# Performance work log

Hardware: AMD Instinct MI355X
Metric: run time of the kernel (lower is better)

## Reference

```python
import jax, jax.numpy as jnp
import numpy as np

B, C, H, W = 8, 64, 256, 256
K = 3  # num_experts in CondConv2D


def setup_inputs() -> dict:
    key = jax.random.key(0)
    ks = jax.random.split(key, 10)
    s = 0.05
    return {
        "x":    jax.random.normal(ks[0], (B, C, H, W), jnp.float32),
        # CondConv2D #1: depthwise 5x5, pad 2, dil 1
        "w0":   jax.random.normal(ks[1], (K, C, 1, 5, 5), jnp.float32) * s,
        "b0":   jax.random.normal(ks[2], (C,), jnp.float32) * s,
        "r0_w": jax.random.normal(ks[3], (K, C), jnp.float32) * s,
        "r0_b": jnp.zeros((K,), jnp.float32),
        # CondConv2D #2: depthwise 7x7, pad 9, dil 3
        "w1":   jax.random.normal(ks[4], (K, C, 1, 7, 7), jnp.float32) * s,
        "b1":   jax.random.normal(ks[5], (C,), jnp.float32) * s,
        "r1_w": jax.random.normal(ks[6], (K, C), jnp.float32) * s,
        "r1_b": jnp.zeros((K,), jnp.float32),
        # conv1: 1x1 pointwise
        "wp":   jax.random.normal(ks[7], (C, C), jnp.float32) * s,
        "bp":   jnp.zeros((C,), jnp.float32),
    }


def cond_dwconv(x, weight, bias, rw, rb, pad, dil):
    """Per-sample expert-mixed depthwise conv (CondConv with groups=C).
    x: [B,C,H,W]; weight: [K,C,1,ks,ks]; rw: [K,C], rb: [K]."""
    b, c, h, w = x.shape
    pooled = x.mean(axis=(2, 3))                      # [B,C] adaptive avg pool to 1x1
    r = jax.nn.sigmoid(pooled @ rw.T + rb)            # [B,K] routing weights
    wk = jnp.einsum('bk,kcihw->bcihw', r, weight)     # [B,C,1,ks,ks] mixed kernels
    ksz = weight.shape[-1]
    # batch-folded grouped conv: fold B into channel/group dim
    out = jax.lax.conv_general_dilated(
        x.reshape(1, b * c, h, w),
        wk.reshape(b * c, 1, ksz, ksz),
        window_strides=(1, 1),
        padding=[(pad, pad), (pad, pad)],
        rhs_dilation=(dil, dil),
        feature_group_count=b * c,
        dimension_numbers=('NCHW', 'OIHW', 'NCHW'))
    return out.reshape(b, c, h, w) + bias[None, :, None, None]


def reference(x, w0, b0, r0_w, r0_b, w1, b1, r1_w, r1_b, wp, bp):
    attn = jax.nn.gelu(cond_dwconv(x, w0, b0, r0_w, r0_b, pad=2, dil=1), approximate=False)
    attn = jax.nn.gelu(cond_dwconv(attn, w1, b1, r1_w, r1_b, pad=9, dil=3), approximate=False)
    attn = jnp.einsum('bchw,oc->bohw', attn, wp) + bp[None, :, None, None]  # 1x1 conv
    return x * attn
```

## Files before the change

### kernel.cpp

```cpp
#include <hip/hip_runtime.h>
#include <hip/hip_fp16.h>

#define HW 65536
#define PW 256
#define C7SD 85

__device__ __forceinline__ float gelu_f(float v) {
    float ax = fabsf(v) * 0.7071067811865476f;
    float t  = 1.0f / (1.0f + 0.3275911f * ax);
    float p  = t * (0.254829592f + t * (-0.284496736f + t * (1.421413741f
             + t * (-1.453152027f + t * 1.061405429f))));
    float e  = 1.0f - p * __expf(-ax * ax);
    e = copysignf(e, v);
    return 0.5f * v * (1.0f + e);
}

__device__ __forceinline__ unsigned pack2h(float a, float b) {
    __half2 h = __floats2half2_rn(a, b);
    return *reinterpret_cast<unsigned*>(&h);
}

__device__ __forceinline__ float sgpr_f(float v) {
    union { float f; int i; } u;
    u.f = v;
    u.i = __builtin_amdgcn_readfirstlane(u.i);
    return u.f;
}

__device__ __forceinline__ void fma_mix_h(float& acc, float w, unsigned h2, int sel) {
    if (sel == 0)
        asm("v_fma_mix_f32 %0, %1, %2, %0 op_sel:[0,0,0] op_sel_hi:[0,1,0]"
            : "+v"(acc) : "v"(w), "v"(h2));
    else
        asm("v_fma_mix_f32 %0, %1, %2, %0 op_sel:[0,1,0] op_sel_hi:[0,1,0]"
            : "+v"(acc) : "v"(w), "v"(h2));
}

__device__ __forceinline__ void dot2_h(float& acc, unsigned wpk, unsigned pr) {
    asm("v_dot2_f32_f16 %0, %1, %2, %0" : "+v"(acc) : "s"(wpk), "v"(pr));
}
__device__ __forceinline__ void dot2_hv(float& acc, unsigned wpk, unsigned pr) {
    asm("v_dot2_f32_f16 %0, %1, %2, %0" : "+v"(acc) : "v"(wpk), "v"(pr));
}

__global__ __launch_bounds__(256) void k_pool_x(const float* __restrict__ x,
                                                float* __restrict__ partial) {
    __shared__ float red[256];
    const int t = threadIdx.x;
    const int blk = blockIdx.x;
    const float* p = x + (size_t)blk * 16384;
    float s = 0.f;
    #pragma unroll
    for (int i = 0; i < 16; ++i) {
        float4 v = *reinterpret_cast<const float4*>(p + (i * 256 + t) * 4);
        s += v.x + v.y + v.z + v.w;
    }
    red[t] = s;
    __syncthreads();
    for (int off = 128; off > 0; off >>= 1) {
        if (t < off) red[t] += red[t + off];
        __syncthreads();
    }
    if (t == 0) partial[blk] = red[0];
}

__device__ __forceinline__ void route_block(const float* __restrict__ partial,
                                            const float* __restrict__ rw,
                                            const float* __restrict__ rb,
                                            const float* __restrict__ wexp,
                                            int b, int c, int taps, int t,
                                            float* pool_s, float* r_s, float* w_s) {
    if (t < 64) {
        float s = 0.f;
        #pragma unroll
        for (int q = 0; q < 4; ++q) s += partial[(b * 64 + t) * 4 + q];
        pool_s[t] = s * (1.0f / 65536.0f);
    }
    __syncthreads();
    if (t < 3) {
        float z = rb[t];
        #pragma unroll
        for (int i = 0; i < 64; ++i) z += pool_s[i] * rw[t * 64 + i];
        r_s[t] = 1.0f / (1.0f + expf(-z));
    }
    __syncthreads();
    if (t < taps) {
        w_s[t] = r_s[0] * wexp[(0 * 64 + c) * taps + t] +
                 r_s[1] * wexp[(1 * 64 + c) * taps + t] +
                 r_s[2] * wexp[(2 * 64 + c) * taps + t];
    }
    __syncthreads();
}

__global__ __launch_bounds__(256) void k_conv5(const float* __restrict__ x,
                                               const float* __restrict__ partial,
                                               const float* __restrict__ rw,
                                               const float* __restrict__ rb,
                                               const float* __restrict__ wexp,
                                               const float* __restrict__ bias,
                                               __half* __restrict__ attn0,
                                               float* __restrict__ tilesum) {
    __shared__ float red[256];
    __shared__ float pool_s[64];
    __shared__ float r_s[3];
    __shared__ float w_s[25];
    const int blk = blockIdx.x;
    const int plane = blk >> 2;
    const int tile = blk & 3;
    const int b = plane >> 6;
    const int c = plane & 63;
    const int oy0 = (tile >> 1) << 7;
    const int ox0 = (tile & 1) << 7;
    const int t = threadIdx.x;
    const int ox = ox0 + ((t & 15) << 3);
    const int oy = oy0 + ((t >> 4) << 3);
    const float* xp = x + (size_t)plane * HW;

    route_block(partial, rw, rb, wexp, b, c, 25, t, pool_s, r_s, w_s);
    float w[25];
    #pragma unroll
    for (int i = 0; i < 25; ++i) w[i] = sgpr_f(w_s[i]);

    float acc[8][8];
    #pragma unroll
    for (int i = 0; i < 8; ++i)
        #pragma unroll
        for (int j = 0; j < 8; ++j) acc[i][j] = 0.f;

    #pragma unroll
    for (int r = 0; r < 12; ++r) {
        const int gy = oy - 2 + r;
        if (gy >= 0 && gy < 256) {
            const float* rp = xp + gy * PW + ox;
            float buf[16];
            float4 v;
            if (ox > 0) v = *reinterpret_cast<const float4*>(rp - 4);
            else        v = make_float4(0.f, 0.f, 0.f, 0.f);
            buf[0] = v.x; buf[1] = v.y; buf[2] = v.z; buf[3] = v.w;
            v = *reinterpret_cast<const float4*>(rp);
            buf[4] = v.x; buf[5] = v.y; buf[6] = v.z; buf[7] = v.w;
            v = *reinterpret_cast<const float4*>(rp + 4);
            buf[8] = v.x; buf[9] = v.y; buf[10] = v.z; buf[11] = v.w;
            if (ox < 248) v = *reinterpret_cast<const float4*>(rp + 8);
            else          v = make_float4(0.f, 0.f, 0.f, 0.f);
            buf[12] = v.x; buf[13] = v.y; buf[14] = v.z; buf[15] = v.w;
            #pragma unroll
            for (int i = 0; i < 8; ++i) {
                const int d = r - i;
                if (d >= 0 && d <= 4) {
                    #pragma unroll
                    for (int dx = 0; dx < 5; ++dx) {
                        const float wv = w[d * 5 + dx];
                        #pragma unroll
                        for (int j = 0; j < 8; ++j)
                            acc[i][j] += wv * buf[j + dx + 2];
                    }
                }
            }
        }
    }
    const float bs = bias[c];
    float lsum = 0.f;
    __half* op = attn0 + (size_t)plane * HW;
    #pragma unroll
    for (int i = 0; i < 8; ++i) {
        float g[8];
        #pragma unroll
        for (int j = 0; j < 8; ++j) {
            g[j] = gelu_f(acc[i][j] + bs);
            lsum += g[j];
        }
        uint4 st;
        st.x = pack2h(g[0], g[1]); st.y = pack2h(g[2], g[3]);
        st.z = pack2h(g[4], g[5]); st.w = pack2h(g[6], g[7]);
        *reinterpret_cast<uint4*>(op + (oy + i) * PW + ox) = st;
    }
    red[t] = lsum;
    __syncthreads();
    for (int off = 128; off > 0; off >>= 1) {
        if (t < off) red[t] += red[t + off];
        __syncthreads();
    }
    if (t == 0) tilesum[blk] = red[0];
}

__global__ __launch_bounds__(256, 3) void k_conv7(const __half* __restrict__ a0,
                                                  const float* __restrict__ tilesum,
                                                  const float* __restrict__ rw,
                                                  const float* __restrict__ rb,
                                                  const float* __restrict__ wexp,
                                                  const float* __restrict__ bias,
                                                  __half* __restrict__ attn1) {
    __shared__ unsigned lds[82 * C7SD];
    __shared__ float pool_s[64];
    __shared__ float r_s[3];
    __shared__ float w_s[49];
    const int blk = blockIdx.x;
    const int plane = blk >> 3;
    const int tile = blk & 7;
    const int b = plane >> 6;
    const int c = plane & 63;
    const int oy0 = (tile >> 1) << 6;
    const int ox0 = (tile & 1) << 7;
    const int t = threadIdx.x;
    const __half* ap = a0 + (size_t)plane * HW;

    const uint4 z4 = make_uint4(0u, 0u, 0u, 0u);
    #pragma unroll
    for (int it = 0; it < 7; ++it) {
        const int idx = it * 256 + t;
        if (idx < 1722) {
            const int lr = idx / 21;
            const int c8 = idx - lr * 21;
            const int gy = oy0 - 9 + lr;
            const int gx = ox0 - 16 + (c8 << 3);
            uint4 v = z4;
            if ((unsigned)gy < 256u && (unsigned)gx < 256u)
                v = *reinterpret_cast<const uint4*>(ap + gy * PW + gx);
            unsigned* wp = &lds[lr * C7SD + (c8 << 2)];
            wp[0] = v.x; wp[1] = v.y; wp[2] = v.z; wp[3] = v.w;
        }
    }

    route_block(tilesum, rw, rb, wexp, b, c, 49, t, pool_s, r_s, w_s);
    unsigned wpk[21];
    #pragma unroll
    for (int p = 0; p < 3; ++p)
        #pragma unroll
        for (int dxi = 0; dxi < 7; ++dxi)
            wpk[p * 7 + dxi] = (unsigned)__builtin_amdgcn_readfirstlane(
                (int)pack2h(w_s[(2 * p) * 7 + dxi], w_s[(2 * p + 1) * 7 + dxi]));
    float wt[7];
    #pragma unroll
    for (int i = 0; i < 7; ++i) wt[i] = sgpr_f(w_s[42 + i]);
    __syncthreads();

    const int tx = t & 3, ty = t >> 2;
    const int ox = tx << 5;
    float acc[32];
    #pragma unroll
    for (int j = 0; j < 32; ++j) acc[j] = 0.f;

    #pragma unroll
    for (int p = 0; p < 3; ++p) {
        const int rA = ty + 6 * p;
        const unsigned* lA = &lds[rA * C7SD + (tx << 4)];
        const unsigned* lB = &lds[(rA + 3) * C7SD + (tx << 4)];
        unsigned hA[32], hB[32];
        #pragma unroll
        for (int i = 0; i < 32; ++i) hA[i] = lA[i];
        #pragma unroll
        for (int i = 0; i < 32; ++i) hB[i] = lB[i];
        unsigned pr[50];
        #pragma unroll
        for (int i = 0; i < 50; ++i) {
            const int s = i + 7, k = s >> 1;
            pr[i] = __builtin_amdgcn_perm(hB[k], hA[k],
                                          (s & 1) ? 0x07060302u : 0x05040100u);
        }
        #pragma unroll
        for (int dxi = 0; dxi < 7; ++dxi) {
            const unsigned wp = wpk[p * 7 + dxi];
            #pragma unroll
            for (int j = 0; j < 32; ++j)
                dot2_h(acc[j], wp, pr[3 * dxi + j]);
        }
    }
    {
        const unsigned* lp = &lds[(ty + 18) * C7SD + (tx << 4)];
        unsigned hbuf[32];
        #pragma unroll
        for (int i = 0; i < 32; ++i) hbuf[i] = lp[i];
        #pragma unroll
        for (int dxi = 0; dxi < 7; ++dxi) {
            const float wv = wt[dxi];
            const int o = 7 + 3 * dxi;
            #pragma unroll
            for (int j = 0; j < 32; ++j) {
                const int h = o + j;
                fma_mix_h(acc[j], wv, hbuf[h >> 1], h & 1);
            }
        }
    }

    const float bs = bias[c];
    __half* op = attn1 + (size_t)plane * HW + (size_t)(oy0 + ty) * PW + ox0 + ox;
    #pragma unroll
    for (int q = 0; q < 4; ++q) {
        float g[8];
        #pragma unroll
        for (int j = 0; j < 8; ++j) g[j] = gelu_f(acc[q * 8 + j] + bs);
        uint4 st;
        st.x = pack2h(g[0], g[1]); st.y = pack2h(g[2], g[3]);
        st.z = pack2h(g[4], g[5]); st.w = pack2h(g[6], g[7]);
        *reinterpret_cast<uint4*>(op + (q << 3)) = st;
    }
}

__global__ __launch_bounds__(256) void k_mix(const __half* __restrict__ attn1,
                                             const float* __restrict__ wpm,
                                             const float* __restrict__ bp,
                                             const float* __restrict__ x,
                                             float* __restrict__ out) {
    __shared__ __half A_s[64][128];
    __shared__ unsigned w2_s[32][64];
    const int t = threadIdx.x;
    const int blk = blockIdx.x;
    const int b = blk >> 9;
    const int p0g = (blk & 511) << 7;
    #pragma unroll
    for (int it = 0; it < 4; ++it) {
        const int idx = it * 256 + t;
        const int row = idx >> 4;
        const int off = (idx & 15) << 3;
        uint4 u = *reinterpret_cast<const uint4*>(attn1 + (size_t)(b * 64 + row) * HW + p0g + off);
        *reinterpret_cast<uint4*>(&A_s[row][off]) = u;
    }
    #pragma unroll
    for (int j = 0; j < 8; ++j) {
        const int idx = j * 256 + t;
        const int oo = idx >> 5;
        const int cc2 = idx & 31;
        w2_s[cc2][oo] = pack2h(wpm[oo * 64 + 2 * cc2], wpm[oo * 64 + 2 * cc2 + 1]);
    }
    __syncthreads();
    const int o0 = (t >> 4) << 2;
    const int p0 = (t & 15) << 3;
    float acc[4][8];
    #pragma unroll
    for (int i = 0; i < 4; ++i)
        #pragma unroll
        for (int j = 0; j < 8; ++j) acc[i][j] = 0.f;
    #pragma unroll 4
    for (int cc2 = 0; cc2 < 32; ++cc2) {
        uint4 a0 = *reinterpret_cast<const uint4*>(&A_s[2 * cc2][p0]);
        uint4 a1 = *reinterpret_cast<const uint4*>(&A_s[2 * cc2 + 1][p0]);
        const unsigned a0w[4] = {a0.x, a0.y, a0.z, a0.w};
        const unsigned a1w[4] = {a1.x, a1.y, a1.z, a1.w};
        unsigned pr[8];
        #pragma unroll
        for (int j = 0; j < 8; ++j)
            pr[j] = __builtin_amdgcn_perm(a1w[j >> 1], a0w[j >> 1],
                                          (j & 1) ? 0x07060302u : 0x05040100u);
        uint4 wv0 = *reinterpret_cast<const uint4*>(&w2_s[cc2][o0]);
        const unsigned wv[4] = {wv0.x, wv0.y, wv0.z, wv0.w};
        #pragma unroll
        for (int oo = 0; oo < 4; ++oo) {
            const unsigned wvv = wv[oo];
            #pragma unroll
            for (int pp = 0; pp < 8; ++pp)
                dot2_hv(acc[oo][pp], wvv, pr[pp]);
        }
    }
    #pragma unroll
    for (int oo = 0; oo < 4; ++oo) {
        const int o = o0 + oo;
        const float bb = bp[o];
        const size_t base = (size_t)(b * 64 + o) * HW + p0g + p0;
        float4 x0 = *reinterpret_cast<const float4*>(x + base);
        float4 x1 = *reinterpret_cast<const float4*>(x + base + 4);
        float4 r0, r1;
        r0.x = x0.x * (acc[oo][0] + bb); r0.y = x0.y * (acc[oo][1] + bb);
        r0.z = x0.z * (acc[oo][2] + bb); r0.w = x0.w * (acc[oo][3] + bb);
        r1.x = x1.x * (acc[oo][4] + bb); r1.y = x1.y * (acc[oo][5] + bb);
        r1.z = x1.z * (acc[oo][6] + bb); r1.w = x1.w * (acc[oo][7] + bb);
        *reinterpret_cast<float4*>(out + base) = r0;
        *reinterpret_cast<float4*>(out + base + 4) = r1;
    }
}

extern "C" void kernel_launch(void* const* d_in, const int* in_sizes, int n_in,
                              void* d_out, int out_size, void* d_ws, size_t ws_size,
                              hipStream_t stream) {
    const float* x   = (const float*)d_in[0];
    const float* w0  = (const float*)d_in[1];
    const float* b0  = (const float*)d_in[2];
    const float* r0w = (const float*)d_in[3];
    const float* r0b = (const float*)d_in[4];
    const float* w1  = (const float*)d_in[5];
    const float* b1  = (const float*)d_in[6];
    const float* r1w = (const float*)d_in[7];
    const float* r1b = (const float*)d_in[8];
    const float* wpm = (const float*)d_in[9];
    const float* bp  = (const float*)d_in[10];
    float* out = (float*)d_out;

    char* ws = (char*)d_ws;
    __half* attn0   = (__half*)(ws);
    __half* attn1   = (__half*)(ws + 67108864);
    float* partial0 = (float*)(ws + 134217728);
    float* tilesum1 = (float*)(ws + 134217728 + 8192);

    k_pool_x<<<2048, 256, 0, stream>>>(x, partial0);
    k_conv5<<<2048, 256, 0, stream>>>(x, partial0, r0w, r0b, w0, b0, attn0, tilesum1);
    k_conv7<<<4096, 256, 0, stream>>>(attn0, tilesum1, r1w, r1b, w1, b1, attn1);
    k_mix<<<4096, 256, 0, stream>>>(attn1, wpm, bp, x, out);
}
```

Before: 227.7 us.

## Rewrite 5x5 conv to stage fp16 tiles in LDS and use packed dot2

```diff
diff --git a/kernel.cpp b/kernel.cpp
--- a/kernel.cpp
+++ b/kernel.cpp
@@ -4,6 +4,7 @@
 #define HW 65536
 #define PW 256
 #define C7SD 85
+#define C5SD 73
 
 __device__ __forceinline__ float gelu_f(float v) {
     float ax = fabsf(v) * 0.7071067811865476f;
@@ -68,12 +69,11 @@
                                             const float* __restrict__ rw,
                                             const float* __restrict__ rb,
                                             const float* __restrict__ wexp,
-                                            int b, int c, int taps, int t,
+                                            int b, int c, int taps, int parts, int t,
                                             float* pool_s, float* r_s, float* w_s) {
     if (t < 64) {
         float s = 0.f;
-        #pragma unroll
-        for (int q = 0; q < 4; ++q) s += partial[(b * 64 + t) * 4 + q];
+        for (int q = 0; q < parts; ++q) s += partial[(b * 64 + t) * parts + q];
         pool_s[t] = s * (1.0f / 65536.0f);
     }
     __syncthreads();
@@ -92,88 +92,126 @@
     __syncthreads();
 }
 
-__global__ __launch_bounds__(256) void k_conv5(const float* __restrict__ x,
-                                               const float* __restrict__ partial,
-                                               const float* __restrict__ rw,
-                                               const float* __restrict__ rb,
-                                               const float* __restrict__ wexp,
-                                               const float* __restrict__ bias,
-                                               __half* __restrict__ attn0,
-                                               float* __restrict__ tilesum) {
+__global__ __launch_bounds__(256, 3) void k_conv5(const float* __restrict__ x,
+                                                  const float* __restrict__ partial,
+                                                  const float* __restrict__ rw,
+                                                  const float* __restrict__ rb,
+                                                  const float* __restrict__ wexp,
+                                                  const float* __restrict__ bias,
+                                                  __half* __restrict__ attn0,
+                                                  float* __restrict__ tilesum) {
+    __shared__ unsigned lds[68 * C5SD];
     __shared__ float red[256];
     __shared__ float pool_s[64];
     __shared__ float r_s[3];
     __shared__ float w_s[25];
     const int blk = blockIdx.x;
-    const int plane = blk >> 2;
-    const int tile = blk & 3;
+    const int plane = blk >> 3;
+    const int tile = blk & 7;
     const int b = plane >> 6;
     const int c = plane & 63;
-    const int oy0 = (tile >> 1) << 7;
+    const int oy0 = (tile >> 1) << 6;
     const int ox0 = (tile & 1) << 7;
     const int t = threadIdx.x;
-    const int ox = ox0 + ((t & 15) << 3);
-    const int oy = oy0 + ((t >> 4) << 3);
     const float* xp = x + (size_t)plane * HW;
 
-    route_block(partial, rw, rb, wexp, b, c, 25, t, pool_s, r_s, w_s);
-    float w[25];
-    #pragma unroll
-    for (int i = 0; i < 25; ++i) w[i] = sgpr_f(w_s[i]);
-
-    float acc[8][8];
-    #pragma unroll
-    for (int i = 0; i < 8; ++i)
-        #pragma unroll
-        for (int j = 0; j < 8; ++j) acc[i][j] = 0.f;
-
-    #pragma unroll
-    for (int r = 0; r < 12; ++r) {
-        const int gy = oy - 2 + r;
-        if (gy >= 0 && gy < 256) {
-            const float* rp = xp + gy * PW + ox;
-            float buf[16];
-            float4 v;
-            if (ox > 0) v = *reinterpret_cast<const float4*>(rp - 4);
-            else        v = make_float4(0.f, 0.f, 0.f, 0.f);
-            buf[0] = v.x; buf[1] = v.y; buf[2] = v.z; buf[3] = v.w;
-            v = *reinterpret_cast<const float4*>(rp);
-            buf[4] = v.x; buf[5] = v.y; buf[6] = v.z; buf[7] = v.w;
-            v = *reinterpret_cast<const float4*>(rp + 4);
-            buf[8] = v.x; buf[9] = v.y; buf[10] = v.z; buf[11] = v.w;
-            if (ox < 248) v = *reinterpret_cast<const float4*>(rp + 8);
-            else          v = make_float4(0.f, 0.f, 0.f, 0.f);
-            buf[12] = v.x; buf[13] = v.y; buf[14] = v.z; buf[15] = v.w;
-            #pragma unroll
-            for (int i = 0; i < 8; ++i) {
-                const int d = r - i;
-                if (d >= 0 && d <= 4) {
-                    #pragma unroll
-                    for (int dx = 0; dx < 5; ++dx) {
-                        const float wv = w[d * 5 + dx];
-                        #pragma unroll
-                        for (int j = 0; j < 8; ++j)
-                            acc[i][j] += wv * buf[j + dx + 2];
-                    }
+    #pragma unroll
+    for (int it = 0; it < 5; ++it) {
+        const int idx = it * 256 + t;
+        if (idx < 1224) {
+            const int lr = idx / 18;
+            const int c8 = idx - lr * 18;
+            const int gy = oy0 - 2 + lr;
+            const int gx = ox0 - 8 + (c8 << 3);
+            unsigned d0 = 0u, d1 = 0u, d2 = 0u, d3 = 0u;
+            if ((unsigned)gy < 256u) {
+                if ((unsigned)gx < 256u) {
+                    float4 v = *reinterpret_cast<const float4*>(xp + gy * PW + gx);
+                    d0 = pack2h(v.x, v.y); d1 = pack2h(v.z, v.w);
+                }
+                if ((unsigned)(gx + 4) < 256u) {
+                    float4 v = *reinterpret_cast<const float4*>(xp + gy * PW + gx + 4);
+                    d2 = pack2h(v.x, v.y); d3 = pack2h(v.z, v.w);
                 }
             }
-        }
-    }
+            unsigned* wp = &lds[lr * C5SD + (c8 << 2)];
+            wp[0] = d0; wp[1] = d1; wp[2] = d2; wp[3] = d3;
+        }
+    }
+
+    route_block(partial, rw, rb, wexp, b, c, 25, 4, t, pool_s, r_s, w_s);
+    unsigned wpk[10];
+    #pragma unroll
+    for (int p = 0; p < 2; ++p)
+        #pragma unroll
+        for (int dx = 0; dx < 5; ++dx)
+            wpk[p * 5 + dx] = (unsigned)__builtin_amdgcn_readfirstlane(
+                (int)pack2h(w_s[(2 * p) * 5 + dx], w_s[(2 * p + 1) * 5 + dx]));
+    float wt[5];
+    #pragma unroll
+    for (int i = 0; i < 5; ++i) wt[i] = sgpr_f(w_s[20 + i]);
+    __syncthreads();
+
+    const int tx = t & 3, ty = t >> 2;
+    const int ox = tx << 5;
+    float acc[32];
+    #pragma unroll
+    for (int j = 0; j < 32; ++j) acc[j] = 0.f;
+
+    #pragma unroll
+    for (int p = 0; p < 2; ++p) {
+        const int lrA = ty + 2 * p;
+        const unsigned* lA = &lds[lrA * C5SD + (tx << 4) + 3];
+        const unsigned* lB = &lds[(lrA + 1) * C5SD + (tx << 4) + 3];
+        unsigned hA[19], hB[19];
+        #pragma unroll
+        for (int i = 0; i < 19; ++i) hA[i] = lA[i];
+        #pragma unroll
+        for (int i = 0; i < 19; ++i) hB[i] = lB[i];
+        unsigned pr[37];
+        #pragma unroll
+        for (int q = 0; q < 37; ++q)
+            pr[q] = __builtin_amdgcn_perm(hB[q >> 1], hA[q >> 1],
+                                          (q & 1) ? 0x07060302u : 0x05040100u);
+        #pragma unroll
+        for (int dx = 0; dx < 5; ++dx) {
+            const unsigned wp = wpk[p * 5 + dx];
+            #pragma unroll
+            for (int j = 0; j < 32; ++j)
+                dot2_h(acc[j], wp, pr[j + dx]);
+        }
+    }
+    {
+        const unsigned* lp = &lds[(ty + 4) * C5SD + (tx << 4) + 3];
+        unsigned hbuf[19];
+        #pragma unroll
+        for (int i = 0; i < 19; ++i) hbuf[i] = lp[i];
+        #pragma unroll
+        for (int dx = 0; dx < 5; ++dx) {
+            const float wv = wt[dx];
+            #pragma unroll
+            for (int j = 0; j < 32; ++j) {
+                const int q = j + dx;
+                fma_mix_h(acc[j], wv, hbuf[q >> 1], q & 1);
+            }
+        }
+    }
+
     const float bs = bias[c];
     float lsum = 0.f;
-    __half* op = attn0 + (size_t)plane * HW;
-    #pragma unroll
-    for (int i = 0; i < 8; ++i) {
+    __half* op = attn0 + (size_t)plane * HW + (size_t)(oy0 + ty) * PW + ox0 + ox;
+    #pragma unroll
+    for (int q = 0; q < 4; ++q) {
         float g[8];
         #pragma unroll
         for (int j = 0; j < 8; ++j) {
-            g[j] = gelu_f(acc[i][j] + bs);
+            g[j] = gelu_f(acc[q * 8 + j] + bs);
             lsum += g[j];
         }
         uint4 st;
         st.x = pack2h(g[0], g[1]); st.y = pack2h(g[2], g[3]);
         st.z = pack2h(g[4], g[5]); st.w = pack2h(g[6], g[7]);
-        *reinterpret_cast<uint4*>(op + (oy + i) * PW + ox) = st;
+        *reinterpret_cast<uint4*>(op + (q << 3)) = st;
     }
     red[t] = lsum;
     __syncthreads();
@@ -222,7 +260,7 @@
         }
     }
 
-    route_block(tilesum, rw, rb, wexp, b, c, 49, t, pool_s, r_s, w_s);
+    route_block(tilesum, rw, rb, wexp, b, c, 49, 8, t, pool_s, r_s, w_s);
     unsigned wpk[21];
     #pragma unroll
     for (int p = 0; p < 3; ++p)
@@ -389,10 +427,10 @@
     __half* attn0   = (__half*)(ws);
     __half* attn1   = (__half*)(ws + 67108864);
     float* partial0 = (float*)(ws + 134217728);
-    float* tilesum1 = (float*)(ws + 134217728 + 8192);
+    float* tilesum1 = (float*)(ws + 134217728 + 16384);
 
     k_pool_x<<<2048, 256, 0, stream>>>(x, partial0);
-    k_conv5<<<2048, 256, 0, stream>>>(x, partial0, r0w, r0b, w0, b0, attn0, tilesum1);
+    k_conv5<<<4096, 256, 0, stream>>>(x, partial0, r0w, r0b, w0, b0, attn0, tilesum1);
     k_conv7<<<4096, 256, 0, stream>>>(attn0, tilesum1, r1w, r1b, w1, b1, attn1);
     k_mix<<<4096, 256, 0, stream>>>(attn1, wpm, bp, x, out);
 }
```

Measured after the change: 227.7 us. No clear change (+0.0%).
